# Optimization experiments

Measured on AMD Instinct MI355X. Metric: run time of the kernel, lower is better.

Reference implementation:

```python
import jax, jax.numpy as jnp
import numpy as np

N = 50000
E = 800000
D = 128
H = 8
DH = D // H


def setup_inputs() -> dict:
    key = jax.random.key(0)
    ks = jax.random.split(key, 8)
    x = jax.random.normal(ks[0], (N, D), dtype=jnp.float32)
    src = jax.random.randint(ks[1], (E,), 0, N, dtype=jnp.int32)
    dst = jax.random.randint(ks[2], (E,), 0, N, dtype=jnp.int32)
    s = 1.0 / np.sqrt(D)
    w_qkv = jax.random.uniform(ks[3], (3 * D, D), jnp.float32, -s, s)
    b_qkv = jax.random.uniform(ks[4], (3 * D,), jnp.float32, -s, s)
    w_out = jax.random.uniform(ks[5], (D, D), jnp.float32, -s, s)
    b_out = jax.random.uniform(ks[6], (D,), jnp.float32, -s, s)
    return {"x": x, "src": src, "dst": dst, "w_qkv": w_qkv, "b_qkv": b_qkv,
            "w_out": w_out, "b_out": b_out}


def reference(x, src, dst, w_qkv, b_qkv, w_out, b_out):
    n = x.shape[0]
    coef = 1.0 / np.sqrt(DH)
    qkv = (x @ w_qkv.T + b_qkv).reshape(n, H, 3 * DH)
    q, k, v = qkv[..., :DH], qkv[..., DH:2 * DH], qkv[..., 2 * DH:]
    # per-edge scores: dot(k[src], q[dst]) per head -> [E, H]
    scores = jnp.einsum('ehd,ehd->eh', k[src], q[dst]) * coef
    # edge softmax over edges sharing the same destination node
    smax = jax.ops.segment_max(scores, dst, num_segments=n)  # [N, H]
    smax = jnp.where(jnp.isfinite(smax), smax, 0.0)
    ex = jnp.exp(scores - smax[dst])                          # [E, H]
    denom = jax.ops.segment_sum(ex, dst, num_segments=n)      # [N, H]
    probs = ex / jnp.maximum(denom[dst], 1e-30)
    # weighted aggregation of source values -> [N, H, DH]
    agg = jax.ops.segment_sum(probs[:, :, None] * v[src], dst, num_segments=n)
    out = agg.reshape(n, D) @ w_out.T + b_out
    return out
```

## Files before the change

### kernel.cpp

```cpp
#include <hip/hip_runtime.h>
#include <math.h>

#define DD   128
#define NQKV 384
#define CAP  128

typedef __attribute__((ext_vector_type(8))) short          bf16x8;
typedef __attribute__((ext_vector_type(8))) unsigned short ushort8;
typedef __attribute__((ext_vector_type(4))) float          f32x4;

__device__ __forceinline__ unsigned short f2bf(float f) {
    unsigned u = __float_as_uint(f);
    u += 0x7fffu + ((u >> 16) & 1u);
    return (unsigned short)(u >> 16);
}
__device__ __forceinline__ float bf2f(unsigned short h) {
    return __uint_as_float(((unsigned)h) << 16);
}
__device__ __forceinline__ float bflo(unsigned u) { return __uint_as_float(u << 16); }
__device__ __forceinline__ float bfhi(unsigned u) { return __uint_as_float(u & 0xffff0000u); }

#define NWQ8 (NQKV * DD / 8)
#define NWO8 (DD * DD / 8)

__global__ void prep_kernel(const float* __restrict__ x,
                            const float* __restrict__ w_qkv, const float* __restrict__ w_out,
                            unsigned short* __restrict__ xbf,
                            unsigned short* __restrict__ wq_hi, unsigned short* __restrict__ wq_lo,
                            unsigned short* __restrict__ wo_hi, unsigned short* __restrict__ wo_lo,
                            int* __restrict__ counts, int nzc4, int nx8) {
    int i = blockIdx.x * blockDim.x + threadIdx.x;
    if (i < nzc4) {
        ((int4*)counts)[i] = make_int4(0, 0, 0, 0);
        return;
    }
    int j = i - nzc4;
    if (j >= NWQ8 + NWO8) {
        int k = j - NWQ8 - NWO8;
        if (k >= nx8) return;
        const float4* p = (const float4*)(x + (size_t)k * 8);
        float4 a = p[0], b = p[1];
        float v[8] = {a.x, a.y, a.z, a.w, b.x, b.y, b.z, b.w};
        ushort8 vh;
        #pragma unroll
        for (int t = 0; t < 8; ++t) vh[t] = f2bf(v[t]);
        *(ushort8*)(xbf + (size_t)k * 8) = vh;
        return;
    }
    const float* srcp;
    unsigned short *hip_, *lop_;
    if (j < NWQ8)            { srcp = w_qkv + (size_t)j * 8;          hip_ = wq_hi + (size_t)j * 8;          lop_ = wq_lo + (size_t)j * 8; }
    else                     { int k = j - NWQ8; srcp = w_out + (size_t)k * 8; hip_ = wo_hi + (size_t)k * 8; lop_ = wo_lo + (size_t)k * 8; }
    const float4* p = (const float4*)srcp;
    float4 a = p[0], b = p[1];
    float v[8] = {a.x, a.y, a.z, a.w, b.x, b.y, b.z, b.w};
    ushort8 vh, vl;
    #pragma unroll
    for (int t = 0; t < 8; ++t) {
        unsigned short h = f2bf(v[t]);
        vh[t] = h;
        vl[t] = f2bf(v[t] - bf2f(h));
    }
    *(ushort8*)hip_ = vh;
    *(ushort8*)lop_ = vl;
}

__global__ void scatter_fixed_kernel(const int* __restrict__ src, const int* __restrict__ dst,
                                     int* __restrict__ counts, int* __restrict__ lists, int E) {
    int t = blockIdx.x * blockDim.x + threadIdx.x;
    int base = t * 8;
    if (base >= E) return;
    if (base + 8 <= E) {
        int4 d0 = *(const int4*)(dst + base);
        int4 d1 = *(const int4*)(dst + base + 4);
        int4 s0 = *(const int4*)(src + base);
        int4 s1 = *(const int4*)(src + base + 4);
        int dd[8] = {d0.x, d0.y, d0.z, d0.w, d1.x, d1.y, d1.z, d1.w};
        int ss[8] = {s0.x, s0.y, s0.z, s0.w, s1.x, s1.y, s1.z, s1.w};
        int pos[8];
        #pragma unroll
        for (int i = 0; i < 8; ++i) pos[i] = atomicAdd(&counts[dd[i]], 1);
        #pragma unroll
        for (int i = 0; i < 8; ++i)
            if (pos[i] < CAP) lists[(size_t)dd[i] * CAP + pos[i]] = ss[i];
    } else {
        for (int e = base; e < E; ++e) {
            int d = dst[e];
            int pos = atomicAdd(&counts[d], 1);
            if (pos < CAP) lists[(size_t)d * CAP + pos] = src[e];
        }
    }
}

#define TM 128
#define TN 128
#define GY_QKV 170
#define GX_OUT 196

__global__ __launch_bounds__(256, 2) void qkv_gemm_kernel(
    const unsigned short* __restrict__ Xb,
    const unsigned short* __restrict__ Bh, const unsigned short* __restrict__ Bl,
    const float* __restrict__ bias, unsigned short* __restrict__ Cq,
    unsigned short* __restrict__ Ck, unsigned short* __restrict__ Cv,
    int M, int mtiles)
{
    __shared__ unsigned short BsH[TN * DD];
    __shared__ unsigned short BsL[TN * DD];

    const int tid  = threadIdx.x;
    const int l    = tid & 63;
    const int wv   = tid >> 6;
    const int quad = l >> 4;
    const int l15  = l & 15;
    const int wm   = (wv & 1) * 64;
    const int wn   = (wv >> 1) * 64;
    const int n0   = blockIdx.x * TN;

    const size_t gbase = (size_t)n0 * DD;
    for (int i = tid; i < TN * 16; i += 256) {
        int col = i >> 4, g = i & 15;
        int gs  = g ^ (col & 15);
        *(ushort8*)&BsH[col * DD + gs * 8] = *(const ushort8*)(Bh + gbase + (size_t)col * DD + g * 8);
        *(ushort8*)&BsL[col * DD + gs * 8] = *(const ushort8*)(Bl + gbase + (size_t)col * DD + g * 8);
    }
    __syncthreads();

    for (int mt0 = blockIdx.y; mt0 < mtiles; mt0 += gridDim.y) {
        const int m0 = mt0 * TM;

        f32x4 acc[4][4];
        #pragma unroll
        for (int i = 0; i < 4; ++i)
            #pragma unroll
            for (int j = 0; j < 4; ++j) acc[i][j] = (f32x4)0.f;

        bf16x8 af[4][4];
        #pragma unroll
        for (int mt = 0; mt < 4; ++mt) {
            const unsigned short* ar = Xb + (size_t)(m0 + wm + mt * 16 + l15) * DD + quad * 8;
            #pragma unroll
            for (int kq = 0; kq < 4; ++kq) af[mt][kq] = *(const bf16x8*)(ar + kq * 32);
        }

        #pragma unroll
        for (int kq = 0; kq < 4; ++kq) {
            bf16x8 bh[4], bl[4];
            #pragma unroll
            for (int nt = 0; nt < 4; ++nt) {
                int colL = wn + nt * 16 + l15;
                int gs   = (kq * 4 + quad) ^ (colL & 15);
                bh[nt] = *(const bf16x8*)&BsH[colL * DD + gs * 8];
                bl[nt] = *(const bf16x8*)&BsL[colL * DD + gs * 8];
            }
            #pragma unroll
            for (int mt = 0; mt < 4; ++mt)
                #pragma unroll
                for (int nt = 0; nt < 4; ++nt) {
                    acc[mt][nt] = __builtin_amdgcn_mfma_f32_16x16x32_bf16(af[mt][kq], bh[nt], acc[mt][nt], 0, 0, 0);
                    acc[mt][nt] = __builtin_amdgcn_mfma_f32_16x16x32_bf16(af[mt][kq], bl[nt], acc[mt][nt], 0, 0, 0);
                }
        }

        #pragma unroll
        for (int nt = 0; nt < 4; ++nt) {
            int j = n0 + wn + nt * 16 + l15;
            float bj = bias[j];
            int h = j / 48;
            int r = j - h * 48;
            int seg = (r >= 32) ? 2 : ((r >= 16) ? 1 : 0);
            int bc  = h * 16 + r - seg * 16;
            unsigned short* dstp = (seg == 0 ? Cq : (seg == 1 ? Ck : Cv));
            #pragma unroll
            for (int mt = 0; mt < 4; ++mt)
                #pragma unroll
                for (int rr = 0; rr < 4; ++rr) {
                    int m = m0 + wm + mt * 16 + quad * 4 + rr;
                    if (m < M) dstp[(size_t)m * DD + bc] = f2bf(acc[mt][nt][rr] + bj);
                }
        }
    }
}

__global__ __launch_bounds__(256, 2) void out_gemm_kernel(
    const unsigned short* __restrict__ A,
    const unsigned short* __restrict__ Bh, const unsigned short* __restrict__ Bl,
    const float* __restrict__ bias, float* __restrict__ C, int M, int mtiles)
{
    __shared__ unsigned short BsH[TN * DD];
    __shared__ unsigned short BsL[TN * DD];

    const int tid  = threadIdx.x;
    const int l    = tid & 63;
    const int wv   = tid >> 6;
    const int quad = l >> 4;
    const int l15  = l & 15;
    const int wm   = (wv & 1) * 64;
    const int wn   = (wv >> 1) * 64;

    for (int i = tid; i < TN * 16; i += 256) {
        int col = i >> 4, g = i & 15;
        int gs  = g ^ (col & 15);
        *(ushort8*)&BsH[col * DD + gs * 8] = *(const ushort8*)(Bh + (size_t)col * DD + g * 8);
        *(ushort8*)&BsL[col * DD + gs * 8] = *(const ushort8*)(Bl + (size_t)col * DD + g * 8);
    }
    __syncthreads();

    for (int mt0 = blockIdx.x; mt0 < mtiles; mt0 += gridDim.x) {
        const int m0 = mt0 * TM;

        f32x4 acc[4][4];
        #pragma unroll
        for (int i = 0; i < 4; ++i)
            #pragma unroll
            for (int j = 0; j < 4; ++j) acc[i][j] = (f32x4)0.f;

        bf16x8 af[4][4];
        #pragma unroll
        for (int mt = 0; mt < 4; ++mt) {
            const unsigned short* ar = A + (size_t)(m0 + wm + mt * 16 + l15) * DD + quad * 8;
            #pragma unroll
            for (int kq = 0; kq < 4; ++kq) af[mt][kq] = *(const bf16x8*)(ar + kq * 32);
        }

        #pragma unroll
        for (int kq = 0; kq < 4; ++kq) {
            bf16x8 bh[4], bl[4];
            #pragma unroll
            for (int nt = 0; nt < 4; ++nt) {
                int colL = wn + nt * 16 + l15;
                int gs   = (kq * 4 + quad) ^ (colL & 15);
                bh[nt] = *(const bf16x8*)&BsH[colL * DD + gs * 8];
                bl[nt] = *(const bf16x8*)&BsL[colL * DD + gs * 8];
            }
            #pragma unroll
            for (int mt = 0; mt < 4; ++mt)
                #pragma unroll
                for (int nt = 0; nt < 4; ++nt) {
                    acc[mt][nt] = __builtin_amdgcn_mfma_f32_16x16x32_bf16(af[mt][kq], bh[nt], acc[mt][nt], 0, 0, 0);
                    acc[mt][nt] = __builtin_amdgcn_mfma_f32_16x16x32_bf16(af[mt][kq], bl[nt], acc[mt][nt], 0, 0, 0);
                }
        }

        #pragma unroll
        for (int nt = 0; nt < 4; ++nt) {
            int j = wn + nt * 16 + l15;
            float bj = bias[j];
            #pragma unroll
            for (int mt = 0; mt < 4; ++mt)
                #pragma unroll
                for (int rr = 0; rr < 4; ++rr) {
                    int m = m0 + wm + mt * 16 + quad * 4 + rr;
                    if (m < M) C[(size_t)m * DD + j] = acc[mt][nt][rr] + bj;
                }
        }
    }
}

#define ATTN_BLOCKS 2048

#define ATTN_STEP(cka, ckb, cvv, nka, nkb, nvv)                                   \
  {                                                                                \
    const int cnt  = min(8, deg - c);                                              \
    const bool more = (c + 8 < deg);                                               \
    const int nn = lists[row0 + min(c + 16 + e, deg - 1)];                         \
    if (more) {                                                                    \
      const unsigned koff = (((unsigned)nxt) << 8) + hoff;                         \
      nka = *(const uint4*)(kb8 + koff);                                           \
      nkb = *(const uint4*)(kb8 + koff + 16);                                      \
      _Pragma("unroll")                                                            \
      for (int ee = 0; ee < 8; ++ee)                                               \
        nvv[ee] = *(const unsigned*)(vb8 + ((((unsigned)__shfl(nxt, ee)) << 8) + loff4)); \
    }                                                                              \
                                           \
    float sA = bflo(cka.x) * q0.x;                                                 \
    sA = fmaf(bfhi(cka.x), q0.y, sA);                                              \
    sA = fmaf(bflo(cka.y), q0.z, sA);                                              \
    sA = fmaf(bfhi(cka.y), q0.w, sA);                                              \
    float sB = bflo(cka.z) * q1.x;                                                 \
    sB = fmaf(bfhi(cka.z), q1.y, sB);                                              \
    sB = fmaf(bflo(cka.w), q1.z, sB);                                              \
    sB = fmaf(bfhi(cka.w), q1.w, sB);                                              \
    float sC = bflo(ckb.x) * q2.x;                                                 \
    sC = fmaf(bfhi(ckb.x), q2.y, sC);                                              \
    sC = fmaf(bflo(ckb.y), q2.z, sC);                                              \
    sC = fmaf(bfhi(ckb.y), q2.w, sC);                                              \
    float sD = bflo(ckb.z) * q3.x;                                                 \
    sD = fmaf(bfhi(ckb.z), q3.y, sD);                                              \
    sD = fmaf(bflo(ckb.w), q3.z, sD);                                              \
    sD = fmaf(bfhi(ckb.w), q3.w, sD);                                              \
    const float s_ = (sA + sB) + (sC + sD);                                        \
    const float pp = __expf(s_ * 0.25f);                           \
    const float p_ = (e < cnt) ? pp : 0.f;                                         \
    l_run += p_;                                                                   \
    _Pragma("unroll")                                                              \
    for (int ee = 0; ee < 8; ++ee) {                                               \
      const float pe = __shfl(p_, lbase | ee);          \
      if ((ee & 1) == 0) {                                                         \
        acc0a = fmaf(pe, bflo(cvv[ee]), acc0a);                                    \
        acc1a = fmaf(pe, bfhi(cvv[ee]), acc1a);                                    \
      } else {                                                                     \
        acc0b = fmaf(pe, bflo(cvv[ee]), acc0b);                                    \
        acc1b = fmaf(pe, bfhi(cvv[ee]), acc1b);                                    \
      }                                                                            \
    }                                                                              \
    nxt = nn;                                                                      \
    c += 8;                                                                        \
  }

__global__ __launch_bounds__(256) void wave_attn_kernel(
    const unsigned short* __restrict__ qbf, const unsigned short* __restrict__ kbf,
    const unsigned short* __restrict__ vbf, const int* __restrict__ lists,
    const int* __restrict__ counts,
    unsigned short* __restrict__ agg, int N)
{
    const int lane   = threadIdx.x & 63;
    const int wid    = blockIdx.x * 4 + (threadIdx.x >> 6);
    const int nwaves = gridDim.x * 4;

    const int h = lane >> 3;
    const int e = lane & 7;
    const unsigned hoff  = (unsigned)h << 5;
    const unsigned loff4 = (unsigned)lane << 2;
    const int lbase = lane & 0x38;

    const char* kb8 = (const char*)kbf;
    const char* vb8 = (const char*)vbf;
    const char* qb8 = (const char*)qbf;
    char*       ab8 = (char*)agg;

    for (int n = wid; n < N; n += nwaves) {
        const int deg = min(counts[n], CAP);
        const unsigned ooff = (((unsigned)n) << 8) + loff4;
        if (deg == 0) {
            *(unsigned*)(ab8 + ooff) = 0u;
            continue;
        }

        const int row0 = n * CAP;

        const unsigned qoff = (((unsigned)n) << 8) + hoff;
        const uint4 qa = *(const uint4*)(qb8 + qoff);
        const uint4 qb = *(const uint4*)(qb8 + qoff + 16);
        const float4 q0 = make_float4(bflo(qa.x), bfhi(qa.x), bflo(qa.y), bfhi(qa.y));
        const float4 q1 = make_float4(bflo(qa.z), bfhi(qa.z), bflo(qa.w), bfhi(qa.w));
        const float4 q2 = make_float4(bflo(qb.x), bfhi(qb.x), bflo(qb.y), bfhi(qb.y));
        const float4 q3 = make_float4(bflo(qb.z), bfhi(qb.z), bflo(qb.w), bfhi(qb.w));

        const int c0s = lists[row0 + min(e, deg - 1)];
        int nxt = lists[row0 + min(8 + e, deg - 1)];

        uint4 ka0, kb0, ka1, kb1;
        unsigned vv0[8], vv1[8];
        {
            const unsigned koff = (((unsigned)c0s) << 8) + hoff;
            ka0 = *(const uint4*)(kb8 + koff);
            kb0 = *(const uint4*)(kb8 + koff + 16);
            #pragma unroll
            for (int ee = 0; ee < 8; ++ee)
                vv0[ee] = *(const unsigned*)(vb8 + ((((unsigned)__shfl(c0s, ee)) << 8) + loff4));
        }
        ka1 = ka0; kb1 = kb0;
        #pragma unroll
        for (int ee = 0; ee < 8; ++ee) vv1[ee] = 0u;

        float l_run = 0.f;
        float acc0a = 0.f, acc0b = 0.f, acc1a = 0.f, acc1b = 0.f;

        int c = 0;
        for (;;) {
            ATTN_STEP(ka0, kb0, vv0, ka1, kb1, vv1);
            if (c >= deg) break;
            ATTN_STEP(ka1, kb1, vv1, ka0, kb0, vv0);
            if (c >= deg) break;
        }

        l_run += __shfl_xor(l_run, 1);
        l_run += __shfl_xor(l_run, 2);
        l_run += __shfl_xor(l_run, 4);

        const float inv = 1.f / fmaxf(l_run, 1e-30f);
        const float o0 = (acc0a + acc0b) * inv, o1 = (acc1a + acc1b) * inv;
        *(unsigned*)(ab8 + ooff) = (unsigned)f2bf(o0) | ((unsigned)f2bf(o1) << 16);
    }
}

extern "C" void kernel_launch(void* const* d_in, const int* in_sizes, int n_in,
                              void* d_out, int out_size, void* d_ws, size_t ws_size,
                              hipStream_t stream) {
    const float* x     = (const float*)d_in[0];
    const int*   src   = (const int*)  d_in[1];
    const int*   dst   = (const int*)  d_in[2];
    const float* w_qkv = (const float*)d_in[3];
    const float* b_qkv = (const float*)d_in[4];
    const float* w_out = (const float*)d_in[5];
    const float* b_out = (const float*)d_in[6];
    float* out = (float*)d_out;

    const int N = in_sizes[0] / DD;
    const int E = in_sizes[1];

    typedef unsigned short u16;
    char* ws = (char*)d_ws;
    u16* qbf   = (u16*)ws;   ws += (size_t)N * DD * sizeof(u16);
    u16* kbf   = (u16*)ws;   ws += (size_t)N * DD * sizeof(u16);
    u16* vbf   = (u16*)ws;   ws += (size_t)N * DD * sizeof(u16);
    u16* aggb  = (u16*)ws;   ws += (size_t)N * DD * sizeof(u16);
    u16* wq_hi = (u16*)ws;   ws += (size_t)NQKV * DD * sizeof(u16);
    u16* wq_lo = (u16*)ws;   ws += (size_t)NQKV * DD * sizeof(u16);
    u16* wo_hi = (u16*)ws;   ws += (size_t)DD * DD * sizeof(u16);
    u16* wo_lo = (u16*)ws;   ws += (size_t)DD * DD * sizeof(u16);
    int* counts = (int*)ws;  ws += (size_t)((N + 3) / 4 * 4) * sizeof(int);
    int* lists  = (int*)ws;  ws += (size_t)N * CAP * sizeof(int);

    u16* xbf = aggb;

    const int nx8  = N * DD / 8;
    const int nzc4 = (N + 3) / 4;
    const int npb  = (nzc4 + NWQ8 + NWO8 + nx8 + 255) / 256;
    const int nsb  = ((E + 7) / 8 + 255) / 256;
    const int MB   = (N + TM - 1) / TM;

    prep_kernel<<<npb, 256, 0, stream>>>(x, w_qkv, w_out, xbf,
                                         wq_hi, wq_lo, wo_hi, wo_lo,
                                         counts, nzc4, nx8);
    scatter_fixed_kernel<<<nsb, 256, 0, stream>>>(src, dst, counts, lists, E);

    qkv_gemm_kernel<<<dim3(NQKV / TN, GY_QKV), 256, 0, stream>>>(
        xbf, wq_hi, wq_lo, b_qkv, qbf, kbf, vbf, N, MB);

    wave_attn_kernel<<<ATTN_BLOCKS, 256, 0, stream>>>(
        qbf, kbf, vbf, lists, counts, aggb, N);

    out_gemm_kernel<<<GX_OUT, 256, 0, stream>>>(
        aggb, wo_hi, wo_lo, b_out, out, N, MB);
}
```

Baseline: 227.4 us.

## Use head-major Q and interleaved KV layout with per-head attention blocks

The QKV GEMM now writes Q in a head-major [H][N][16] layout and K/V interleaved per head as [H][N][32], so a head's key and value for one node share a 64-byte row. The attention kernel assigns each block to a single head, with each wave handling 8 nodes at once (one per 8-lane group), padding loops to the group's maximum degree. The aim is to shrink the per-head gather working set so it fits in cache better and to fetch K and V from the same line. The cost is extra wasted iterations on low-degree nodes within a group, and the output GEMM now gathers A rows from a head-major agg layout, which is less contiguous.

```diff
diff --git a/kernel.cpp b/kernel.cpp
--- a/kernel.cpp
+++ b/kernel.cpp
@@ -101,7 +101,7 @@
     const unsigned short* __restrict__ Xb,
     const unsigned short* __restrict__ Bh, const unsigned short* __restrict__ Bl,
     const float* __restrict__ bias, unsigned short* __restrict__ Cq,
-    unsigned short* __restrict__ Ck, unsigned short* __restrict__ Cv,
+    unsigned short* __restrict__ Ckv,
     int M, int mtiles)
 {
     __shared__ unsigned short BsH[TN * DD];
@@ -168,14 +168,18 @@
             int h = j / 48;
             int r = j - h * 48;
             int seg = (r >= 32) ? 2 : ((r >= 16) ? 1 : 0);
-            int bc  = h * 16 + r - seg * 16;
-            unsigned short* dstp = (seg == 0 ? Cq : (seg == 1 ? Ck : Cv));
+            int dim = r - seg * 16;
+            const bool isq = (seg == 0);
+            unsigned short* dstp = isq ? Cq : Ckv;
+            const int rs   = isq ? 16 : 32;
+            const int off0 = dim + ((seg == 2) ? 16 : 0);
+            const size_t hb = (size_t)h * M;
             #pragma unroll
             for (int mt = 0; mt < 4; ++mt)
                 #pragma unroll
                 for (int rr = 0; rr < 4; ++rr) {
                     int m = m0 + wm + mt * 16 + quad * 4 + rr;
-                    if (m < M) dstp[(size_t)m * DD + bc] = f2bf(acc[mt][nt][rr] + bj);
+                    if (m < M) dstp[(hb + m) * rs + off0] = f2bf(acc[mt][nt][rr] + bj);
                 }
         }
     }
@@ -217,9 +221,15 @@
         bf16x8 af[4][4];
         #pragma unroll
         for (int mt = 0; mt < 4; ++mt) {
-            const unsigned short* ar = A + (size_t)(m0 + wm + mt * 16 + l15) * DD + quad * 8;
-            #pragma unroll
-            for (int kq = 0; kq < 4; ++kq) af[mt][kq] = *(const bf16x8*)(ar + kq * 32);
+            const int mrow = m0 + wm + mt * 16 + l15;
+            const int mclamp = (mrow < M) ? mrow : (M - 1);
+            #pragma unroll
+            for (int kq = 0; kq < 4; ++kq) {
+                const int d0  = kq * 32 + quad * 8;
+                const int hh  = d0 >> 4;
+                const int off = d0 & 15;
+                af[mt][kq] = *(const bf16x8*)(A + ((size_t)hh * M + mclamp) * 16 + off);
+            }
         }
 
         #pragma unroll
@@ -260,18 +270,18 @@
 
 #define ATTN_STEP(cka, ckb, cvv, nka, nkb, nvv)                                   \
   {                                                                                \
-    const int cnt  = min(8, deg - c);                                              \
-    const bool more = (c + 8 < deg);                                               \
-    const int nn = lists[row0 + min(c + 16 + e, deg - 1)];                         \
+    const bool more = (c + 8 < maxdeg);                                            \
+    int nn = lists[lrow + min(c + 16 + e, degc - 1)];                              \
+    if (deg <= 0) nn = 0;                                                          \
     if (more) {                                                                    \
-      const unsigned koff = (((unsigned)nxt) << 8) + hoff;                         \
-      nka = *(const uint4*)(kb8 + koff);                                           \
-      nkb = *(const uint4*)(kb8 + koff + 16);                                      \
+      const unsigned koff = ((unsigned)nxt) << 6;                                  \
+      nka = *(const uint4*)(kvb + koff);                                           \
+      nkb = *(const uint4*)(kvb + koff + 16);                                      \
       _Pragma("unroll")                                                            \
       for (int ee = 0; ee < 8; ++ee)                                               \
-        nvv[ee] = *(const unsigned*)(vb8 + ((((unsigned)__shfl(nxt, ee)) << 8) + loff4)); \
+        nvv[ee] = *(const unsigned*)(kvb + ((((unsigned)__shfl(nxt, lbase | ee)) << 6) + voff)); \
     }                                                                              \
-                                           \
+                     \
     float sA = bflo(cka.x) * q0.x;                                                 \
     sA = fmaf(bfhi(cka.x), q0.y, sA);                                              \
     sA = fmaf(bflo(cka.y), q0.z, sA);                                              \
@@ -289,8 +299,7 @@
     sD = fmaf(bflo(ckb.w), q3.z, sD);                                              \
     sD = fmaf(bfhi(ckb.w), q3.w, sD);                                              \
     const float s_ = (sA + sB) + (sC + sD);                                        \
-    const float pp = __expf(s_ * 0.25f);                           \
-    const float p_ = (e < cnt) ? pp : 0.f;                                         \
+    const float p_ = (c + e < deg) ? __expf(s_ * 0.25f) : 0.f;     \
     l_run += p_;                                                                   \
     _Pragma("unroll")                                                              \
     for (int ee = 0; ee < 8; ++ee) {                                               \
@@ -308,56 +317,60 @@
   }
 
 __global__ __launch_bounds__(256) void wave_attn_kernel(
-    const unsigned short* __restrict__ qbf, const unsigned short* __restrict__ kbf,
-    const unsigned short* __restrict__ vbf, const int* __restrict__ lists,
-    const int* __restrict__ counts,
-    unsigned short* __restrict__ agg, int N)
+    const unsigned short* __restrict__ qhm,
+    const unsigned short* __restrict__ kvm,
+    const int* __restrict__ lists, const int* __restrict__ counts,
+    unsigned short* __restrict__ agg,
+    int N)
 {
-    const int lane   = threadIdx.x & 63;
-    const int wid    = blockIdx.x * 4 + (threadIdx.x >> 6);
-    const int nwaves = gridDim.x * 4;
-
-    const int h = lane >> 3;
-    const int e = lane & 7;
-    const unsigned hoff  = (unsigned)h << 5;
-    const unsigned loff4 = (unsigned)lane << 2;
+    const int lane = threadIdx.x & 63;
+    const int head = blockIdx.x & 7;
+    const int wid  = (blockIdx.x >> 3) * 4 + (threadIdx.x >> 6);
+    const int nwph = (gridDim.x >> 3) * 4;
+
+    const int ns = lane >> 3;
+    const int e  = lane & 7;
     const int lbase = lane & 0x38;
-
-    const char* kb8 = (const char*)kbf;
-    const char* vb8 = (const char*)vbf;
-    const char* qb8 = (const char*)qbf;
-    char*       ab8 = (char*)agg;
-
-    for (int n = wid; n < N; n += nwaves) {
-        const int deg = min(counts[n], CAP);
-        const unsigned ooff = (((unsigned)n) << 8) + loff4;
-        if (deg == 0) {
-            *(unsigned*)(ab8 + ooff) = 0u;
-            continue;
-        }
-
-        const int row0 = n * CAP;
-
-        const unsigned qoff = (((unsigned)n) << 8) + hoff;
-        const uint4 qa = *(const uint4*)(qb8 + qoff);
-        const uint4 qb = *(const uint4*)(qb8 + qoff + 16);
-        const float4 q0 = make_float4(bflo(qa.x), bfhi(qa.x), bflo(qa.y), bfhi(qa.y));
-        const float4 q1 = make_float4(bflo(qa.z), bfhi(qa.z), bflo(qa.w), bfhi(qa.w));
-        const float4 q2 = make_float4(bflo(qb.x), bfhi(qb.x), bflo(qb.y), bfhi(qb.y));
-        const float4 q3 = make_float4(bflo(qb.z), bfhi(qb.z), bflo(qb.w), bfhi(qb.w));
-
-        const int c0s = lists[row0 + min(e, deg - 1)];
-        int nxt = lists[row0 + min(8 + e, deg - 1)];
+    const unsigned voff = 32u + ((unsigned)e << 2);
+
+    const char* kvb = (const char*)kvm + ((size_t)head * N) * 64;
+    const char* qpb = (const char*)qhm + ((size_t)head * N) * 32;
+    char*       ab  = (char*)agg + ((size_t)head * N) * 32;
+
+    const int ngroups = (N + 7) >> 3;
+    for (int g = wid; g < ngroups; g += nwph) {
+        const int node  = g * 8 + ns;
+        const int nodec = min(node, N - 1);
+        const int deg   = (node < N) ? min(counts[nodec], CAP) : 0;
+        const int degc  = max(deg, 1);
+        int maxdeg = deg;
+        maxdeg = max(maxdeg, __shfl_xor(maxdeg, 8));
+        maxdeg = max(maxdeg, __shfl_xor(maxdeg, 16));
+        maxdeg = max(maxdeg, __shfl_xor(maxdeg, 32));
+
+        const int lrow = nodec * CAP;
+
+        const unsigned qoff = ((unsigned)nodec) << 5;
+        const uint4 qw0 = *(const uint4*)(qpb + qoff);
+        const uint4 qw1 = *(const uint4*)(qpb + qoff + 16);
+        const float4 q0 = make_float4(bflo(qw0.x), bfhi(qw0.x), bflo(qw0.y), bfhi(qw0.y));
+        const float4 q1 = make_float4(bflo(qw0.z), bfhi(qw0.z), bflo(qw0.w), bfhi(qw0.w));
+        const float4 q2 = make_float4(bflo(qw1.x), bfhi(qw1.x), bflo(qw1.y), bfhi(qw1.y));
+        const float4 q3 = make_float4(bflo(qw1.z), bfhi(qw1.z), bflo(qw1.w), bfhi(qw1.w));
+
+        int cur = lists[lrow + min(e, degc - 1)];
+        int nxt = lists[lrow + min(8 + e, degc - 1)];
+        if (deg <= 0) { cur = 0; nxt = 0; }
 
         uint4 ka0, kb0, ka1, kb1;
         unsigned vv0[8], vv1[8];
         {
-            const unsigned koff = (((unsigned)c0s) << 8) + hoff;
-            ka0 = *(const uint4*)(kb8 + koff);
-            kb0 = *(const uint4*)(kb8 + koff + 16);
+            const unsigned koff = ((unsigned)cur) << 6;
+            ka0 = *(const uint4*)(kvb + koff);
+            kb0 = *(const uint4*)(kvb + koff + 16);
             #pragma unroll
             for (int ee = 0; ee < 8; ++ee)
-                vv0[ee] = *(const unsigned*)(vb8 + ((((unsigned)__shfl(c0s, ee)) << 8) + loff4));
+                vv0[ee] = *(const unsigned*)(kvb + ((((unsigned)__shfl(cur, lbase | ee)) << 6) + voff));
         }
         ka1 = ka0; kb1 = kb0;
         #pragma unroll
@@ -367,11 +380,10 @@
         float acc0a = 0.f, acc0b = 0.f, acc1a = 0.f, acc1b = 0.f;
 
         int c = 0;
-        for (;;) {
+        while (c < maxdeg) {
             ATTN_STEP(ka0, kb0, vv0, ka1, kb1, vv1);
-            if (c >= deg) break;
+            if (c >= maxdeg) break;
             ATTN_STEP(ka1, kb1, vv1, ka0, kb0, vv0);
-            if (c >= deg) break;
         }
 
         l_run += __shfl_xor(l_run, 1);
@@ -380,7 +392,9 @@
 
         const float inv = 1.f / fmaxf(l_run, 1e-30f);
         const float o0 = (acc0a + acc0b) * inv, o1 = (acc1a + acc1b) * inv;
-        *(unsigned*)(ab8 + ooff) = (unsigned)f2bf(o0) | ((unsigned)f2bf(o1) << 16);
+        if (node < N)
+            *(unsigned*)(ab + (((unsigned)g) << 8) + ((unsigned)lane << 2)) =
+                (unsigned)f2bf(o0) | ((unsigned)f2bf(o1) << 16);
     }
 }
 
@@ -402,8 +416,7 @@
     typedef unsigned short u16;
     char* ws = (char*)d_ws;
     u16* qbf   = (u16*)ws;   ws += (size_t)N * DD * sizeof(u16);
-    u16* kbf   = (u16*)ws;   ws += (size_t)N * DD * sizeof(u16);
-    u16* vbf   = (u16*)ws;   ws += (size_t)N * DD * sizeof(u16);
+    u16* kvbuf = (u16*)ws;   ws += (size_t)N * DD * 2 * sizeof(u16);
     u16* aggb  = (u16*)ws;   ws += (size_t)N * DD * sizeof(u16);
     u16* wq_hi = (u16*)ws;   ws += (size_t)NQKV * DD * sizeof(u16);
     u16* wq_lo = (u16*)ws;   ws += (size_t)NQKV * DD * sizeof(u16);
@@ -426,10 +439,10 @@
     scatter_fixed_kernel<<<nsb, 256, 0, stream>>>(src, dst, counts, lists, E);
 
     qkv_gemm_kernel<<<dim3(NQKV / TN, GY_QKV), 256, 0, stream>>>(
-        xbf, wq_hi, wq_lo, b_qkv, qbf, kbf, vbf, N, MB);
+        xbf, wq_hi, wq_lo, b_qkv, qbf, kvbuf, N, MB);
 
     wave_attn_kernel<<<ATTN_BLOCKS, 256, 0, stream>>>(
-        qbf, kbf, vbf, lists, counts, aggb, N);
+        qbf, kvbuf, lists, counts, aggb, N);
 
     out_gemm_kernel<<<GX_OUT, 256, 0, stream>>>(
         aggb, wo_hi, wo_lo, b_out, out, N, MB);
```

Measured after the change: 244.1 us. 1.07x slower.
